# Kernel optimization log

Hardware: AMD Instinct MI355X
Metric: run time of the kernel (lower is better)

## Reference

```python
import jax, jax.numpy as jnp
import numpy as np


def _conv1d_same(x, k):
    # x: [N, L, Cin], k: [K, Cin, Cout] (flax Conv layout), stride 1, SAME padding
    return jax.lax.conv_general_dilated(
        x, k, window_strides=(1,), padding='SAME',
        dimension_numbers=('NWC', 'WIO', 'NWC'))


def setup_inputs() -> dict:
    key = jax.random.key(0)
    ks = jax.random.split(key, 5)
    B, T, L, C, H, OUT = 16, 64, 512, 64, 150, 24
    xs = jax.random.normal(ks[0], (B, T, L, C), jnp.float32)
    # small init scale to keep gates out of saturation
    ki = jax.random.normal(ks[1], (5, C, 3 * H), jnp.float32) * 0.05
    kh = jax.random.normal(ks[2], (5, H, 3 * H), jnp.float32) * 0.05
    W1 = jax.random.normal(ks[3], (H, H), jnp.float32) * 0.08
    b1 = jnp.zeros((H,), jnp.float32)
    W2 = jax.random.normal(ks[4], (H, OUT), jnp.float32) * 0.08
    b2 = jnp.zeros((OUT,), jnp.float32)
    return {"xs": xs, "ki": ki, "kh": kh, "W1": W1, "b1": b1, "W2": W2, "b2": b2}


def reference(xs, ki, kh, W1, b1, W2, b2):
    B, T, L, C = xs.shape
    H = kh.shape[1]
    # input-to-gates conv for all timesteps at once: [B*T, L, C] -> [B, T, L, 3H]
    gates_i = _conv1d_same(xs.reshape(B * T, L, C), ki).reshape(B, T, L, 3 * H)

    def step(h, gi):
        gh = _conv1d_same(h, kh)                      # [B, L, 3H]
        iir, iiz, iin = jnp.split(gi, 3, axis=-1)
        hir, hiz, hin = jnp.split(gh, 3, axis=-1)
        r = jax.nn.sigmoid(iir + hir)
        z = jax.nn.sigmoid(iiz + hiz)
        n = jnp.tanh(iin + r * hin)
        new_h = (1.0 - z) * n + z * h
        return new_h, new_h

    h0 = jnp.zeros((B, L, H), xs.dtype)
    _, hs = jax.lax.scan(step, h0, jnp.moveaxis(gates_i, 1, 0))  # hs: [T, B, L, H]
    last = hs[-1]                                     # out[:, -1, :] -> [B, L, H]
    hdn = last @ W1 + b1
    hdn = hdn * jax.nn.sigmoid(hdn)                   # silu
    out = hdn @ W2 + b2                               # [B, L, 24]
    return jnp.expand_dims(out, axis=-1)              # [B, L, 24, 1]
```

## Files before the change

### kernel.cpp

```cpp
#include <hip/hip_runtime.h>


#define Bn   16
#define Tn   64
#define Ln   512
#define Cn   64
#define Hn   150
#define G3   450
#define SW   160
#define HP   160
#define KCH  25
#define KCX  10
#define Mtot 8192

typedef __bf16 bf16x8 __attribute__((ext_vector_type(8)));
typedef float  f32x4  __attribute__((ext_vector_type(4)));
typedef short  s16x4  __attribute__((ext_vector_type(4)));

__device__ inline short f2bf(float f) {
  unsigned u = __builtin_bit_cast(unsigned, f);
  u += 0x7fffu + ((u >> 16) & 1u);
  return (short)(u >> 16);
}

__global__ __launch_bounds__(256) void pack_weights(const float* __restrict__ ki,
                                                    const float* __restrict__ kh,
                                                    short* __restrict__ Bx,
                                                    short* __restrict__ Bh) {
  int idx = blockIdx.x * 256 + threadIdx.x;
  if (idx < 32 * KCH * 512) {
    int j = idx & 7, lane = (idx >> 3) & 63;
    int rest = idx >> 9;
    int kc = rest % KCH, nt = rest / KCH;
    int quad = lane >> 4, l16 = lane & 15;
    int n = nt * 16 + l16, seg = n / SW, jl = n - seg * SW;
    int kk = kc / 5, jj = (kc - kk * 5) * 32 + quad * 8 + j;
    float v = (seg < 3 && jl < Hn && jj < Hn) ? kh[(kk * Hn + jj) * G3 + seg * Hn + jl] : 0.f;
    Bh[idx] = f2bf(v);
  } else {
    int r = idx - 32 * KCH * 512;
    if (r < 32 * KCX * 512) {
      int j = r & 7, lane = (r >> 3) & 63;
      int rest = r >> 9;
      int kc = rest % KCX, nt = rest / KCX;
      int quad = lane >> 4, l16 = lane & 15;
      int n = nt * 16 + l16, seg = n / SW, jl = n - seg * SW;
      int kk = kc / 2, cc = (kc - kk * 2) * 32 + quad * 8 + j;
      float v = (seg < 3 && jl < Hn) ? ki[(kk * Cn + cc) * G3 + seg * Hn + jl] : 0.f;
      Bx[r] = f2bf(v);
    }
  }
}

__global__ __launch_bounds__(640)
void gru_step(const short* __restrict__ hbin, short* __restrict__ hbout,
              float* __restrict__ hf, const short* __restrict__ Bh,
              const short* __restrict__ Bx, const float* __restrict__ xs, int t) {
  __shared__ short awh[68 * 168];
  __shared__ short awx[68 * 72];
  const int tid   = threadIdx.x;
  const int nhalf = blockIdx.x & 1;
  const int mblk  = blockIdx.x >> 1;
  const int bb    = mblk >> 3;
  const int l0    = (mblk & 7) * 64;

  for (int i = tid; i < 68 * 40; i += 640) {
    int r = i / 40, c4 = (i - r * 40) * 4;
    int l = l0 - 2 + r;
    s16x4 v = {0, 0, 0, 0};
    if (l >= 0 && l < Ln) v = *(const s16x4*)&hbin[((size_t)bb * Ln + l) * HP + c4];
    *(s16x4*)&awh[r * 168 + c4] = v;
  }
  for (int i = tid; i < 68 * 16; i += 640) {
    int r = i >> 4, c4 = (i & 15) * 4;
    int l = l0 - 2 + r;
    s16x4 v = {0, 0, 0, 0};
    if (l >= 0 && l < Ln) {
      f32x4 f = *(const f32x4*)&xs[(((size_t)bb * Tn + t) * Ln + l) * Cn + c4];
      v[0] = f2bf(f[0]); v[1] = f2bf(f[1]); v[2] = f2bf(f[2]); v[3] = f2bf(f[3]);
    }
    *(s16x4*)&awx[r * 72 + c4] = v;
  }
  __syncthreads();

  const int lane = tid & 63, w = tid >> 6;
  const int quad = lane >> 4, l16 = lane & 15;
  const int jt = w % 5, mi = w / 5;

  const short* Bph[3];
  const short* Bpx[3];
#pragma unroll
  for (int g = 0; g < 3; ++g) {
    const int nt = g * 10 + nhalf * 5 + jt;
    Bph[g] = Bh + (size_t)nt * (KCH * 512) + lane * 8;
    Bpx[g] = Bx + (size_t)nt * (KCX * 512) + lane * 8;
  }
  const int arh = (mi * 32 + l16) * 168 + quad * 8;
  const int arx = (mi * 32 + l16) * 72 + quad * 8;

  f32x4 acc[2][3] = {};
  f32x4 axn[2] = {};

  bf16x8 bx[3][3];
#pragma unroll
  for (int s = 0; s < 2; ++s)
#pragma unroll
    for (int g = 0; g < 3; ++g) bx[s][g] = *(const bf16x8*)(Bpx[g] + s * 512);

  bf16x8 bh[4][3];
#pragma unroll
  for (int s = 0; s < 3; ++s)
#pragma unroll
    for (int g = 0; g < 3; ++g) bh[s][g] = *(const bf16x8*)(Bph[g] + s * 512);

#pragma unroll
  for (int kc = 0; kc < KCH; ++kc) {
    const int cur = kc & 3;
    if (kc + 3 < KCH) {
      const int nxt = (kc + 3) & 3;
#pragma unroll
      for (int g = 0; g < 3; ++g)
        bh[nxt][g] = *(const bf16x8*)(Bph[g] + (kc + 3) * 512);
    }
    const int kk = kc / 5, jj = (kc - kk * 5) * 32;
    const short* ar = &awh[arh + kk * 168 + jj];
    bf16x8 a0 = *(const bf16x8*)(ar);
    bf16x8 a1 = *(const bf16x8*)(ar + 16 * 168);
#pragma unroll
    for (int g = 0; g < 3; ++g) {
      acc[0][g] = __builtin_amdgcn_mfma_f32_16x16x32_bf16(a0, bh[cur][g], acc[0][g], 0, 0, 0);
      acc[1][g] = __builtin_amdgcn_mfma_f32_16x16x32_bf16(a1, bh[cur][g], acc[1][g], 0, 0, 0);
    }
  }

#pragma unroll
  for (int kc = 0; kc < KCX; ++kc) {
    const int cur = kc % 3;
    if (kc + 2 < KCX) {
      const int nxt = (kc + 2) % 3;
#pragma unroll
      for (int g = 0; g < 3; ++g)
        bx[nxt][g] = *(const bf16x8*)(Bpx[g] + (kc + 2) * 512);
    }
    const int kk = kc >> 1, jj = (kc & 1) * 32;
    const short* ar = &awx[arx + kk * 72 + jj];
    bf16x8 a0 = *(const bf16x8*)(ar);
    bf16x8 a1 = *(const bf16x8*)(ar + 16 * 72);
    acc[0][0] = __builtin_amdgcn_mfma_f32_16x16x32_bf16(a0, bx[cur][0], acc[0][0], 0, 0, 0);
    acc[1][0] = __builtin_amdgcn_mfma_f32_16x16x32_bf16(a1, bx[cur][0], acc[1][0], 0, 0, 0);
    acc[0][1] = __builtin_amdgcn_mfma_f32_16x16x32_bf16(a0, bx[cur][1], acc[0][1], 0, 0, 0);
    acc[1][1] = __builtin_amdgcn_mfma_f32_16x16x32_bf16(a1, bx[cur][1], acc[1][1], 0, 0, 0);
    axn[0]    = __builtin_amdgcn_mfma_f32_16x16x32_bf16(a0, bx[cur][2], axn[0], 0, 0, 0);
    axn[1]    = __builtin_amdgcn_mfma_f32_16x16x32_bf16(a1, bx[cur][2], axn[1], 0, 0, 0);
  }

  const int j = nhalf * 80 + jt * 16 + l16;
  if (j < Hn) {
#pragma unroll
    for (int f = 0; f < 2; ++f)
#pragma unroll
      for (int r = 0; r < 4; ++r) {
        const int ml = mi * 32 + f * 16 + quad * 4 + r;
        const size_t mrow = (size_t)bb * Ln + l0 + ml;
        float rg = 1.f / (1.f + __expf(-acc[f][0][r]));
        float zg = 1.f / (1.f + __expf(-acc[f][1][r]));
        float xg = axn[f][r] + rg * acc[f][2][r];
        xg = fminf(fmaxf(xg, -15.f), 15.f);
        float e = __expf(2.f * xg);
        float n = (e - 1.f) / (e + 1.f);
        float hn = (1.f - zg) * n + zg * hf[mrow * Hn + j];
        hf[mrow * Hn + j] = hn;
        hbout[mrow * HP + j] = f2bf(hn);
      }
  }
}

__global__ __launch_bounds__(256) void head1(const float* __restrict__ hf,
                                             const float* __restrict__ W1,
                                             const float* __restrict__ b1,
                                             float* __restrict__ hdn) {
  int idx = blockIdx.x * 256 + threadIdx.x;
  if (idx >= Mtot * Hn) return;
  int m = idx / Hn, j = idx - m * Hn;
  const float* hr = hf + (size_t)m * Hn;
  float acc = b1[j];
#pragma unroll 10
  for (int i = 0; i < Hn; ++i) acc = fmaf(hr[i], W1[i * Hn + j], acc);
  hdn[idx] = acc / (1.f + __expf(-acc));
}
__global__ __launch_bounds__(256) void head2(const float* __restrict__ hdn,
                                             const float* __restrict__ W2,
                                             const float* __restrict__ b2,
                                             float* __restrict__ out) {
  int idx = blockIdx.x * 256 + threadIdx.x;
  if (idx >= Mtot * 24) return;
  int m = idx / 24, j = idx - m * 24;
  const float* hr = hdn + (size_t)m * Hn;
  float acc = b2[j];
#pragma unroll 10
  for (int i = 0; i < Hn; ++i) acc = fmaf(hr[i], W2[i * 24 + j], acc);
  out[idx] = acc;
}

extern "C" void kernel_launch(void* const* d_in, const int* in_sizes, int n_in,
                              void* d_out, int out_size, void* d_ws, size_t ws_size,
                              hipStream_t stream) {
  const float* xs = (const float*)d_in[0];
  const float* ki = (const float*)d_in[1];
  const float* kh = (const float*)d_in[2];
  const float* W1 = (const float*)d_in[3];
  const float* b1 = (const float*)d_in[4];
  const float* W2 = (const float*)d_in[5];
  const float* b2 = (const float*)d_in[6];
  float* out = (float*)d_out;

  char* p = (char*)d_ws;
  float* hf  = (float*)p; p += (size_t)Mtot * Hn * 4;
  float* hdn = (float*)p; p += (size_t)Mtot * Hn * 4;
  short* hbA = (short*)p; p += (size_t)Mtot * HP * 2;
  short* hbB = (short*)p; p += (size_t)Mtot * HP * 2;
  short* Bh  = (short*)p; p += (size_t)32 * KCH * 512 * 2;
  short* Bx  = (short*)p; p += (size_t)32 * KCX * 512 * 2;

  hipMemsetAsync(hf, 0, (size_t)Mtot * Hn * 4, stream);
  hipMemsetAsync(hbA, 0, (size_t)Mtot * HP * 2 * 2, stream);
  pack_weights<<<(32 * (KCH + KCX) * 512 + 255) / 256, 256, 0, stream>>>(ki, kh, Bx, Bh);

  for (int t = 0; t < Tn; ++t) {
    short* hin  = (t & 1) ? hbB : hbA;
    short* hout = (t & 1) ? hbA : hbB;
    gru_step<<<256, 640, 0, stream>>>(hin, hout, hf, Bh, Bx, xs, t);
  }
  head1<<<(Mtot * Hn + 255) / 256, 256, 0, stream>>>(hf, W1, b1, hdn);
  head2<<<(Mtot * 24 + 255) / 256, 256, 0, stream>>>(hdn, W2, b2, out);
}
```

Baseline: 1.433 ms.

## Halve GRU step block size and give each wave four M-fragments

Each gru_step block now runs 5 waves instead of 10, and each wave covers all 64 rows (4 M-fragments) for its 16-column slice in every gate. Every B fragment loaded from global memory now feeds 4 row fragments instead of 2, which halves the global weight traffic per block and raises MFMA work per load. The cost is more accumulator registers per wave and fewer waves to hide latency. Launch bounds of (320, 2) are meant to keep two blocks per CU.

Result: slower. 1.703 ms (+18.9%).

```diff
diff --git a/kernel.cpp b/kernel.cpp
--- a/kernel.cpp
+++ b/kernel.cpp
@@ -52,7 +52,7 @@
   }
 }
 
-__global__ __launch_bounds__(640)
+__global__ __launch_bounds__(320, 2)
 void gru_step(const short* __restrict__ hbin, short* __restrict__ hbout,
               float* __restrict__ hf, const short* __restrict__ Bh,
               const short* __restrict__ Bx, const float* __restrict__ xs, int t) {
@@ -64,14 +64,14 @@
   const int bb    = mblk >> 3;
   const int l0    = (mblk & 7) * 64;
 
-  for (int i = tid; i < 68 * 40; i += 640) {
+  for (int i = tid; i < 68 * 40; i += 320) {
     int r = i / 40, c4 = (i - r * 40) * 4;
     int l = l0 - 2 + r;
     s16x4 v = {0, 0, 0, 0};
     if (l >= 0 && l < Ln) v = *(const s16x4*)&hbin[((size_t)bb * Ln + l) * HP + c4];
     *(s16x4*)&awh[r * 168 + c4] = v;
   }
-  for (int i = tid; i < 68 * 16; i += 640) {
+  for (int i = tid; i < 68 * 16; i += 320) {
     int r = i >> 4, c4 = (i & 15) * 4;
     int l = l0 - 2 + r;
     s16x4 v = {0, 0, 0, 0};
@@ -85,21 +85,20 @@
 
   const int lane = tid & 63, w = tid >> 6;
   const int quad = lane >> 4, l16 = lane & 15;
-  const int jt = w % 5, mi = w / 5;
 
   const short* Bph[3];
   const short* Bpx[3];
 #pragma unroll
   for (int g = 0; g < 3; ++g) {
-    const int nt = g * 10 + nhalf * 5 + jt;
+    const int nt = g * 10 + nhalf * 5 + w;
     Bph[g] = Bh + (size_t)nt * (KCH * 512) + lane * 8;
     Bpx[g] = Bx + (size_t)nt * (KCX * 512) + lane * 8;
   }
-  const int arh = (mi * 32 + l16) * 168 + quad * 8;
-  const int arx = (mi * 32 + l16) * 72 + quad * 8;
-
-  f32x4 acc[2][3] = {};
-  f32x4 axn[2] = {};
+  const int arh = l16 * 168 + quad * 8;
+  const int arx = l16 * 72 + quad * 8;
+
+  f32x4 acc[4][3] = {};
+  f32x4 axn[4] = {};
 
   bf16x8 bx[3][3];
 #pragma unroll
@@ -124,13 +123,14 @@
     }
     const int kk = kc / 5, jj = (kc - kk * 5) * 32;
     const short* ar = &awh[arh + kk * 168 + jj];
-    bf16x8 a0 = *(const bf16x8*)(ar);
-    bf16x8 a1 = *(const bf16x8*)(ar + 16 * 168);
-#pragma unroll
-    for (int g = 0; g < 3; ++g) {
-      acc[0][g] = __builtin_amdgcn_mfma_f32_16x16x32_bf16(a0, bh[cur][g], acc[0][g], 0, 0, 0);
-      acc[1][g] = __builtin_amdgcn_mfma_f32_16x16x32_bf16(a1, bh[cur][g], acc[1][g], 0, 0, 0);
-    }
+    bf16x8 a[4];
+#pragma unroll
+    for (int f = 0; f < 4; ++f) a[f] = *(const bf16x8*)(ar + f * 16 * 168);
+#pragma unroll
+    for (int f = 0; f < 4; ++f)
+#pragma unroll
+      for (int g = 0; g < 3; ++g)
+        acc[f][g] = __builtin_amdgcn_mfma_f32_16x16x32_bf16(a[f], bh[cur][g], acc[f][g], 0, 0, 0);
   }
 
 #pragma unroll
@@ -144,23 +144,24 @@
     }
     const int kk = kc >> 1, jj = (kc & 1) * 32;
     const short* ar = &awx[arx + kk * 72 + jj];
-    bf16x8 a0 = *(const bf16x8*)(ar);
-    bf16x8 a1 = *(const bf16x8*)(ar + 16 * 72);
-    acc[0][0] = __builtin_amdgcn_mfma_f32_16x16x32_bf16(a0, bx[cur][0], acc[0][0], 0, 0, 0);
-    acc[1][0] = __builtin_amdgcn_mfma_f32_16x16x32_bf16(a1, bx[cur][0], acc[1][0], 0, 0, 0);
-    acc[0][1] = __builtin_amdgcn_mfma_f32_16x16x32_bf16(a0, bx[cur][1], acc[0][1], 0, 0, 0);
-    acc[1][1] = __builtin_amdgcn_mfma_f32_16x16x32_bf16(a1, bx[cur][1], acc[1][1], 0, 0, 0);
-    axn[0]    = __builtin_amdgcn_mfma_f32_16x16x32_bf16(a0, bx[cur][2], axn[0], 0, 0, 0);
-    axn[1]    = __builtin_amdgcn_mfma_f32_16x16x32_bf16(a1, bx[cur][2], axn[1], 0, 0, 0);
-  }
-
-  const int j = nhalf * 80 + jt * 16 + l16;
+    bf16x8 a[4];
+#pragma unroll
+    for (int f = 0; f < 4; ++f) a[f] = *(const bf16x8*)(ar + f * 16 * 72);
+#pragma unroll
+    for (int f = 0; f < 4; ++f) {
+      acc[f][0] = __builtin_amdgcn_mfma_f32_16x16x32_bf16(a[f], bx[cur][0], acc[f][0], 0, 0, 0);
+      acc[f][1] = __builtin_amdgcn_mfma_f32_16x16x32_bf16(a[f], bx[cur][1], acc[f][1], 0, 0, 0);
+      axn[f]    = __builtin_amdgcn_mfma_f32_16x16x32_bf16(a[f], bx[cur][2], axn[f], 0, 0, 0);
+    }
+  }
+
+  const int j = nhalf * 80 + w * 16 + l16;
   if (j < Hn) {
 #pragma unroll
-    for (int f = 0; f < 2; ++f)
+    for (int f = 0; f < 4; ++f)
 #pragma unroll
       for (int r = 0; r < 4; ++r) {
-        const int ml = mi * 32 + f * 16 + quad * 4 + r;
+        const int ml = f * 16 + quad * 4 + r;
         const size_t mrow = (size_t)bb * Ln + l0 + ml;
         float rg = 1.f / (1.f + __expf(-acc[f][0][r]));
         float zg = 1.f / (1.f + __expf(-acc[f][1][r]));
@@ -229,7 +230,7 @@
   for (int t = 0; t < Tn; ++t) {
     short* hin  = (t & 1) ? hbB : hbA;
     short* hout = (t & 1) ? hbA : hbB;
-    gru_step<<<256, 640, 0, stream>>>(hin, hout, hf, Bh, Bx, xs, t);
+    gru_step<<<256, 320, 0, stream>>>(hin, hout, hf, Bh, Bx, xs, t);
   }
   head1<<<(Mtot * Hn + 255) / 256, 256, 0, stream>>>(hf, W1, b1, hdn);
   head2<<<(Mtot * 24 + 255) / 256, 256, 0, stream>>>(hdn, W2, b2, out);
```
